# Kernel tuning notes

Hardware: AMD Instinct MI355X
Metric: run time of the kernel (lower is better)

## Reference

```python
import jax, jax.numpy as jnp
import numpy as np


def setup_inputs() -> dict:
    key = jax.random.key(0)
    k1, k2, k3, k4 = jax.random.split(key, 4)
    M, K, N = 16384, 1024, 4096
    # int8-range values stored as int32 (A8W8 path; int32 accumulation is identical)
    x = jax.random.randint(k1, (M, K), -128, 128, dtype=jnp.int32)
    weight = jax.random.randint(k2, (N, K), -128, 128, dtype=jnp.int32)
    scale = jax.random.uniform(k3, (N,), dtype=jnp.float32, minval=0.001, maxval=0.01)
    bias = jax.random.randint(k4, (N,), -64, 64, dtype=jnp.int32)
    return {"x": x, "weight": weight, "scale": scale, "bias": bias}


def reference(x, weight, scale, bias):
    # npu_quant_matmul: int32-accumulated matmul of quantized input with
    # weight^T, int32 bias add, then fused per-out-channel dequant scale.
    acc = jnp.matmul(x, weight.T) + bias[None, :]  # [M, N] int32
    return acc.astype(jnp.float32) * scale[None, :]  # dequantized output
```

## Files before the change

### kernel.cpp

```cpp
#include <hip/hip_runtime.h>

typedef __attribute__((ext_vector_type(4))) int int4v;

#define AS1 __attribute__((address_space(1)))
#define AS3 __attribute__((address_space(3)))

#define BAR()   __builtin_amdgcn_s_barrier()
#define LGKM0() asm volatile("s_waitcnt lgkmcnt(0)" ::: "memory")

#define STG_A(sb, rowbase, k0) \
    __builtin_amdgcn_global_load_lds( \
        (const AS1 void*)(aSrcBase + (size_t)(rowbase) * K + (k0)), \
        (AS3 void*)(ldsDestA + (sb) + (rowbase) * 128), 16, 0, 0)
#define STG_B(sb, rowbase, k0) \
    __builtin_amdgcn_global_load_lds( \
        (const AS1 void*)(bSrcBase + (size_t)(rowbase) * K + (k0)), \
        (AS3 void*)(ldsDestB + (sb) + (rowbase) * 128), 16, 0, 0)

#define LDA(mq, sb) \
    { _Pragma("unroll") for (int m = 0; m < 4; ++m) { \
        const int rb = (sb) + ((aRow0 + ((mq) << 6) + (m << 4)) << 7); \
        a[m][0] = *(const int4v*)(ls + rb + colx0); \
        a[m][1] = *(const int4v*)(ls + rb + colx1); } }

#define LDB(nq, sb) \
    { _Pragma("unroll") for (int n = 0; n < 2; ++n) { \
        const int rb = (sb) + 32768 + ((bRow0 + ((nq) << 5) + (n << 4)) << 7); \
        b[(nq)*2 + n][0] = *(const int4v*)(ls + rb + colx0); \
        b[(nq)*2 + n][1] = *(const int4v*)(ls + rb + colx1); } }

#define MMA(mq, nq) \
    { __builtin_amdgcn_s_setprio(1); \
      _Pragma("unroll") for (int m = 0; m < 4; ++m) \
      _Pragma("unroll") for (int n = 0; n < 2; ++n) { \
        acc[(mq)*4 + m][(nq)*2 + n] = __builtin_amdgcn_mfma_i32_16x16x64_i8( \
            a[m][0], b[(nq)*2 + n][0], acc[(mq)*4 + m][(nq)*2 + n], 0, 0, 0); \
        acc[(mq)*4 + m][(nq)*2 + n] = __builtin_amdgcn_mfma_i32_16x16x64_i8( \
            a[m][1], b[(nq)*2 + n][1], acc[(mq)*4 + m][(nq)*2 + n], 0, 0, 0); } \
      __builtin_amdgcn_s_setprio(0); }

__global__ __launch_bounds__(256) void pack_both_kernel(
    const int* __restrict__ x, const int* __restrict__ w,
    int* __restrict__ x8, int* __restrict__ w8, int n4x, int n4w)
{
    int i = blockIdx.x * blockDim.x + threadIdx.x;
    const int stride = gridDim.x * blockDim.x;
    const int tot = n4x + n4w;
    for (; i < tot; i += stride) {
        const bool isx = i < n4x;
        const int4v v = isx ? ((const int4v*)x)[i] : ((const int4v*)w)[i - n4x];
        const int p = (v.x & 255) | ((v.y & 255) << 8) | ((v.z & 255) << 16) | ((v.w & 255) << 24);
        if (isx) x8[i] = p; else w8[i - n4x] = p;
    }
}

__global__ __launch_bounds__(512, 2) void gemm_i8_256(
    const char* __restrict__ A8, const char* __restrict__ B8,
    const float* __restrict__ scale, const int* __restrict__ bias,
    float* __restrict__ out, int M, int N, int K, int nwg_n)
{
    extern __shared__ __attribute__((aligned(16))) char ls[];

    const int tid  = threadIdx.x;
    const int lane = tid & 63;
    const int wid  = tid >> 6;
    const int wr   = wid >> 2;
    const int wc   = wid & 3;
    const int l15  = lane & 15;
    const int hi16 = lane >> 4;

    int wg = blockIdx.x;
    {
        const int nwg = gridDim.x;
        const int q = nwg >> 3, r = nwg & 7;
        const int x = wg & 7, lq = wg >> 3;
        wg = (x < r ? x * (q + 1) : r * (q + 1) + (x - r) * q) + lq;
    }
    const int m0 = (wg / nwg_n) << 8;
    const int n0 = (wg % nwg_n) << 8;

    const int sw    = (l15 & 7) << 4;
    const int colx0 = ((hi16 << 4)) ^ sw;
    const int colx1 = (64 + (hi16 << 4)) ^ sw;
    const int aRow0 = (wr << 7) + l15;
    const int bRow0 = (wc << 6) + l15;

    const int srow  = tid >> 3;
    const int sslot = tid & 7;
    const int scol  = ((sslot ^ (srow & 7)) << 4);
    const char* aSrcBase = A8 + (size_t)(m0 + srow) * K + scol;
    const char* bSrcBase = B8 + (size_t)(n0 + srow) * K + scol;
    char* ldsDestA = ls + srow * 128 + (sslot << 4);
    char* ldsDestB = ls + 32768 + srow * 128 + (sslot << 4);

    int4v acc[8][4];
#pragma unroll
    for (int i = 0; i < 8; ++i)
#pragma unroll
        for (int j = 0; j < 4; ++j)
            acc[i][j] = (int4v){0, 0, 0, 0};

    int4v a[4][2], b[4][2];

    const int nkt = K >> 7;
    const int nit = nkt >> 1;

    STG_A(0, 0, 0);   STG_A(0, 128, 0);
    STG_A(0, 64, 0);  STG_A(0, 192, 0);
    STG_B(0, 0, 0);   STG_B(0, 64, 0);
    STG_B(0, 128, 0); STG_B(0, 192, 0);
    STG_A(65536, 0, 128); STG_A(65536, 128, 128);
    STG_B(65536, 0, 128); STG_B(65536, 64, 128);
    STG_B(65536, 128, 128); STG_B(65536, 192, 128);
    asm volatile("s_waitcnt vmcnt(6)" ::: "memory");
    BAR();

#pragma unroll 1
    for (int it = 0; it < nit; ++it) {
        const int kO1 = (2 * it + 1) << 7;
        const int tE = 2 * it + 2, tO = 2 * it + 3;
        const int kE = tE << 7, kO = tO << 7;
        const bool ok = tE < nkt;

        LDA(0, 0); LDB(0, 0);
        STG_A(65536, 64, kO1); STG_A(65536, 192, kO1);
        BAR(); LGKM0();
        MMA(0, 0);
        BAR();

        LDB(1, 0);
        if (ok) { STG_A(0, 0, kE); STG_A(0, 128, kE); }
        BAR(); LGKM0();
        MMA(0, 1);
        BAR();

        LDA(1, 0);
        if (ok) { STG_B(0, 0, kE); STG_B(0, 64, kE); }
        BAR(); LGKM0();
        MMA(1, 1);
        BAR();

        if (ok) { STG_B(0, 128, kE); STG_B(0, 192, kE); }
        BAR(); LGKM0();
        MMA(1, 0);
        if (ok) { asm volatile("s_waitcnt vmcnt(6)" ::: "memory"); }
        else    { asm volatile("s_waitcnt vmcnt(0)" ::: "memory"); }
        BAR();

        LDA(0, 65536); LDB(0, 65536);
        if (ok) { STG_A(0, 64, kE); STG_A(0, 192, kE); }
        BAR(); LGKM0();
        MMA(0, 0);
        BAR();

        LDB(1, 65536);
        if (ok) { STG_A(65536, 0, kO); STG_A(65536, 128, kO); }
        BAR(); LGKM0();
        MMA(0, 1);
        BAR();

        LDA(1, 65536);
        if (ok) { STG_B(65536, 0, kO); STG_B(65536, 64, kO); }
        BAR(); LGKM0();
        MMA(1, 1);
        BAR();

        if (ok) { STG_B(65536, 128, kO); STG_B(65536, 192, kO); }
        BAR(); LGKM0();
        MMA(1, 0);
        if (ok) { asm volatile("s_waitcnt vmcnt(6)" ::: "memory"); }
        else    { asm volatile("s_waitcnt vmcnt(0)" ::: "memory"); }
        BAR();
    }

    float scl[4]; int bsv[4];
#pragma unroll
    for (int nj = 0; nj < 4; ++nj) {
        const int col = n0 + (wc << 6) + (nj << 4) + l15;
        scl[nj] = scale[col];
        bsv[nj] = bias[col];
    }
#pragma unroll
    for (int mi = 0; mi < 8; ++mi) {
        const int rowb = m0 + (wr << 7) + (mi << 4) + (hi16 << 2);
#pragma unroll
        for (int nj = 0; nj < 4; ++nj) {
            const int col = n0 + (wc << 6) + (nj << 4) + l15;
            float* o = out + (size_t)rowb * N + col;
#pragma unroll
            for (int r = 0; r < 4; ++r)
                o[(size_t)r * N] = (float)(acc[mi][nj][r] + bsv[nj]) * scl[nj];
        }
    }
}

__global__ __launch_bounds__(256) void naive_kernel(
    const int* __restrict__ x, const int* __restrict__ w,
    const float* __restrict__ scale, const int* __restrict__ bias,
    float* __restrict__ out, int M, int N, int K)
{
    size_t idx = (size_t)blockIdx.x * blockDim.x + threadIdx.x;
    const size_t total = (size_t)M * N;
    const size_t stride = (size_t)gridDim.x * blockDim.x;
    for (; idx < total; idx += stride) {
        const int m = (int)(idx / N), n = (int)(idx % N);
        int acc = 0;
        for (int k = 0; k < K; ++k) acc += x[(size_t)m * K + k] * w[(size_t)n * K + k];
        out[idx] = (float)(acc + bias[n]) * scale[n];
    }
}

extern "C" void kernel_launch(void* const* d_in, const int* in_sizes, int n_in,
                              void* d_out, int out_size, void* d_ws, size_t ws_size,
                              hipStream_t stream)
{
    const int*   x     = (const int*)d_in[0];
    const int*   w     = (const int*)d_in[1];
    const float* scale = (const float*)d_in[2];
    const int*   bias  = (const int*)d_in[3];
    float*       out   = (float*)d_out;

    const int N = in_sizes[2];
    const int K = in_sizes[1] / N;
    const int M = in_sizes[0] / K;

    const size_t needA = (size_t)M * K;
    const size_t needB = (size_t)N * K;

    if (ws_size < needA + needB || (M % 256) || (N % 256) || (K % 256)) {
        naive_kernel<<<8192, 256, 0, stream>>>(x, w, scale, bias, out, M, N, K);
        return;
    }

    char* x8 = (char*)d_ws;
    char* w8 = x8 + needA;

    pack_both_kernel<<<2048, 256, 0, stream>>>(x, w, (int*)x8, (int*)w8,
                                               (int)(needA >> 2), (int)(needB >> 2));

    hipFuncSetAttribute((const void*)gemm_i8_256,
                        hipFuncAttributeMaxDynamicSharedMemorySize, 131072);

    const int nwg_n = N / 256;
    const int nwg = (M / 256) * nwg_n;
    gemm_i8_256<<<nwg, 512, 131072, stream>>>(x8, w8, scale, bias, out, M, N, K, nwg_n);
}
```

Before: 127.9 us.

## Make int8 GEMM persistent with a fixed 256-workgroup grid and chunked tile mapping

Turns the GEMM into a persistent kernel. A grid of at most 256 workgroups loops over the 64x16=1024 output tiles, and each tile restarts its prologue inside the loop. It also replaces the XCD-aware remap with a chunked mapping that gives each of 8 groups a contiguous band of M tiles, aiming for better L2 locality per XCD. Because the grid is 256 workgroups on 256 CUs while 131 KB of LDS allows one resident workgroup per CU, the previous overlap from having many queued workgroups is lost. The tile prologue and epilogue are also no longer overlapped with other work.

```diff
diff --git a/kernel.cpp b/kernel.cpp
--- a/kernel.cpp
+++ b/kernel.cpp
@@ -54,10 +54,11 @@
     }
 }
 
-__global__ __launch_bounds__(512, 2) void gemm_i8_256(
+__global__ __launch_bounds__(512, 2) void gemm_i8_256p(
     const char* __restrict__ A8, const char* __restrict__ B8,
     const float* __restrict__ scale, const int* __restrict__ bias,
-    float* __restrict__ out, int M, int N, int K, int nwg_n)
+    float* __restrict__ out, int M, int N, int K,
+    int mTiles, int nTiles, int chunked)
 {
     extern __shared__ __attribute__((aligned(16))) char ls[];
 
@@ -69,16 +70,6 @@
     const int l15  = lane & 15;
     const int hi16 = lane >> 4;
 
-    int wg = blockIdx.x;
-    {
-        const int nwg = gridDim.x;
-        const int q = nwg >> 3, r = nwg & 7;
-        const int x = wg & 7, lq = wg >> 3;
-        wg = (x < r ? x * (q + 1) : r * (q + 1) + (x - r) * q) + lq;
-    }
-    const int m0 = (wg / nwg_n) << 8;
-    const int n0 = (wg % nwg_n) << 8;
-
     const int sw    = (l15 & 7) << 4;
     const int colx0 = ((hi16 << 4)) ^ sw;
     const int colx1 = (64 + (hi16 << 4)) ^ sw;
@@ -88,108 +79,122 @@
     const int srow  = tid >> 3;
     const int sslot = tid & 7;
     const int scol  = ((sslot ^ (srow & 7)) << 4);
-    const char* aSrcBase = A8 + (size_t)(m0 + srow) * K + scol;
-    const char* bSrcBase = B8 + (size_t)(n0 + srow) * K + scol;
     char* ldsDestA = ls + srow * 128 + (sslot << 4);
     char* ldsDestB = ls + 32768 + srow * 128 + (sslot << 4);
 
-    int4v acc[8][4];
-#pragma unroll
-    for (int i = 0; i < 8; ++i)
-#pragma unroll
-        for (int j = 0; j < 4; ++j)
-            acc[i][j] = (int4v){0, 0, 0, 0};
-
-    int4v a[4][2], b[4][2];
-
     const int nkt = K >> 7;
     const int nit = nkt >> 1;
-
-    STG_A(0, 0, 0);   STG_A(0, 128, 0);
-    STG_A(0, 64, 0);  STG_A(0, 192, 0);
-    STG_B(0, 0, 0);   STG_B(0, 64, 0);
-    STG_B(0, 128, 0); STG_B(0, 192, 0);
-    STG_A(65536, 0, 128); STG_A(65536, 128, 128);
-    STG_B(65536, 0, 128); STG_B(65536, 64, 128);
-    STG_B(65536, 128, 128); STG_B(65536, 192, 128);
-    asm volatile("s_waitcnt vmcnt(6)" ::: "memory");
-    BAR();
+    const int nwg = mTiles * nTiles;
+
+    int4v acc[8][4];
+    int4v a[4][2], b[4][2];
+
+    for (int idx = blockIdx.x; idx < nwg; idx += gridDim.x) {
+        int mt, nt;
+        if (chunked) {
+            const int x = idx & 7, c = idx >> 3;
+            mt = x * (mTiles >> 3) + c / nTiles;
+            nt = c % nTiles;
+        } else {
+            mt = idx / nTiles;
+            nt = idx % nTiles;
+        }
+        const int m0 = mt << 8, n0 = nt << 8;
+        const char* aSrcBase = A8 + (size_t)(m0 + srow) * K + scol;
+        const char* bSrcBase = B8 + (size_t)(n0 + srow) * K + scol;
+
+#pragma unroll
+        for (int i = 0; i < 8; ++i)
+#pragma unroll
+            for (int j = 0; j < 4; ++j)
+                acc[i][j] = (int4v){0, 0, 0, 0};
+
+        STG_A(0, 0, 0);   STG_A(0, 128, 0);
+        STG_A(0, 64, 0);  STG_A(0, 192, 0);
+        STG_B(0, 0, 0);   STG_B(0, 64, 0);
+        STG_B(0, 128, 0); STG_B(0, 192, 0);
+        STG_A(65536, 0, 128); STG_A(65536, 128, 128);
+        STG_B(65536, 0, 128); STG_B(65536, 64, 128);
+        STG_B(65536, 128, 128); STG_B(65536, 192, 128);
+        asm volatile("s_waitcnt vmcnt(6)" ::: "memory");
+        BAR();
 
 #pragma unroll 1
-    for (int it = 0; it < nit; ++it) {
-        const int kO1 = (2 * it + 1) << 7;
-        const int tE = 2 * it + 2, tO = 2 * it + 3;
-        const int kE = tE << 7, kO = tO << 7;
-        const bool ok = tE < nkt;
-
-        LDA(0, 0); LDB(0, 0);
-        STG_A(65536, 64, kO1); STG_A(65536, 192, kO1);
-        BAR(); LGKM0();
-        MMA(0, 0);
-        BAR();
-
-        LDB(1, 0);
-        if (ok) { STG_A(0, 0, kE); STG_A(0, 128, kE); }
-        BAR(); LGKM0();
-        MMA(0, 1);
-        BAR();
-
-        LDA(1, 0);
-        if (ok) { STG_B(0, 0, kE); STG_B(0, 64, kE); }
-        BAR(); LGKM0();
-        MMA(1, 1);
-        BAR();
-
-        if (ok) { STG_B(0, 128, kE); STG_B(0, 192, kE); }
-        BAR(); LGKM0();
-        MMA(1, 0);
-        if (ok) { asm volatile("s_waitcnt vmcnt(6)" ::: "memory"); }
-        else    { asm volatile("s_waitcnt vmcnt(0)" ::: "memory"); }
-        BAR();
-
-        LDA(0, 65536); LDB(0, 65536);
-        if (ok) { STG_A(0, 64, kE); STG_A(0, 192, kE); }
-        BAR(); LGKM0();
-        MMA(0, 0);
-        BAR();
-
-        LDB(1, 65536);
-        if (ok) { STG_A(65536, 0, kO); STG_A(65536, 128, kO); }
-        BAR(); LGKM0();
-        MMA(0, 1);
-        BAR();
-
-        LDA(1, 65536);
-        if (ok) { STG_B(65536, 0, kO); STG_B(65536, 64, kO); }
-        BAR(); LGKM0();
-        MMA(1, 1);
-        BAR();
-
-        if (ok) { STG_B(65536, 128, kO); STG_B(65536, 192, kO); }
-        BAR(); LGKM0();
-        MMA(1, 0);
-        if (ok) { asm volatile("s_waitcnt vmcnt(6)" ::: "memory"); }
-        else    { asm volatile("s_waitcnt vmcnt(0)" ::: "memory"); }
-        BAR();
-    }
-
-    float scl[4]; int bsv[4];
-#pragma unroll
-    for (int nj = 0; nj < 4; ++nj) {
-        const int col = n0 + (wc << 6) + (nj << 4) + l15;
-        scl[nj] = scale[col];
-        bsv[nj] = bias[col];
-    }
-#pragma unroll
-    for (int mi = 0; mi < 8; ++mi) {
-        const int rowb = m0 + (wr << 7) + (mi << 4) + (hi16 << 2);
+        for (int it = 0; it < nit; ++it) {
+            const int kO1 = (2 * it + 1) << 7;
+            const int tE = 2 * it + 2, tO = 2 * it + 3;
+            const int kE = tE << 7, kO = tO << 7;
+            const bool ok = tE < nkt;
+
+            LDA(0, 0); LDB(0, 0);
+            STG_A(65536, 64, kO1); STG_A(65536, 192, kO1);
+            BAR(); LGKM0();
+            MMA(0, 0);
+            BAR();
+
+            LDB(1, 0);
+            if (ok) { STG_A(0, 0, kE); STG_A(0, 128, kE); }
+            BAR(); LGKM0();
+            MMA(0, 1);
+            BAR();
+
+            LDA(1, 0);
+            if (ok) { STG_B(0, 0, kE); STG_B(0, 64, kE); }
+            BAR(); LGKM0();
+            MMA(1, 1);
+            BAR();
+
+            if (ok) { STG_B(0, 128, kE); STG_B(0, 192, kE); }
+            BAR(); LGKM0();
+            MMA(1, 0);
+            if (ok) { asm volatile("s_waitcnt vmcnt(6)" ::: "memory"); }
+            else    { asm volatile("s_waitcnt vmcnt(0)" ::: "memory"); }
+            BAR();
+
+            LDA(0, 65536); LDB(0, 65536);
+            if (ok) { STG_A(0, 64, kE); STG_A(0, 192, kE); }
+            BAR(); LGKM0();
+            MMA(0, 0);
+            BAR();
+
+            LDB(1, 65536);
+            if (ok) { STG_A(65536, 0, kO); STG_A(65536, 128, kO); }
+            BAR(); LGKM0();
+            MMA(0, 1);
+            BAR();
+
+            LDA(1, 65536);
+            if (ok) { STG_B(65536, 0, kO); STG_B(65536, 64, kO); }
+            BAR(); LGKM0();
+            MMA(1, 1);
+            BAR();
+
+            if (ok) { STG_B(65536, 128, kO); STG_B(65536, 192, kO); }
+            BAR(); LGKM0();
+            MMA(1, 0);
+            if (ok) { asm volatile("s_waitcnt vmcnt(6)" ::: "memory"); }
+            else    { asm volatile("s_waitcnt vmcnt(0)" ::: "memory"); }
+            BAR();
+        }
+
+        float scl[4]; int bsv[4];
 #pragma unroll
         for (int nj = 0; nj < 4; ++nj) {
             const int col = n0 + (wc << 6) + (nj << 4) + l15;
-            float* o = out + (size_t)rowb * N + col;
-#pragma unroll
-            for (int r = 0; r < 4; ++r)
-                o[(size_t)r * N] = (float)(acc[mi][nj][r] + bsv[nj]) * scl[nj];
+            scl[nj] = scale[col];
+            bsv[nj] = bias[col];
+        }
+#pragma unroll
+        for (int mi = 0; mi < 8; ++mi) {
+            const int rowb = m0 + (wr << 7) + (mi << 4) + (hi16 << 2);
+#pragma unroll
+            for (int nj = 0; nj < 4; ++nj) {
+                const int col = n0 + (wc << 6) + (nj << 4) + l15;
+                float* o = out + (size_t)rowb * N + col;
+#pragma unroll
+                for (int r = 0; r < 4; ++r)
+                    o[(size_t)r * N] = (float)(acc[mi][nj][r] + bsv[nj]) * scl[nj];
+            }
         }
     }
 }
@@ -238,10 +243,13 @@
     pack_both_kernel<<<2048, 256, 0, stream>>>(x, w, (int*)x8, (int*)w8,
                                                (int)(needA >> 2), (int)(needB >> 2));
 
-    hipFuncSetAttribute((const void*)gemm_i8_256,
+    hipFuncSetAttribute((const void*)gemm_i8_256p,
                         hipFuncAttributeMaxDynamicSharedMemorySize, 131072);
 
-    const int nwg_n = N / 256;
-    const int nwg = (M / 256) * nwg_n;
-    gemm_i8_256<<<nwg, 512, 131072, stream>>>(x8, w8, scale, bias, out, M, N, K, nwg_n);
-}
+    const int mTiles = M / 256, nTiles = N / 256;
+    const int nwg = mTiles * nTiles;
+    const int grid = nwg < 256 ? nwg : 256;
+    const int chunked = (mTiles % 8 == 0) ? 1 : 0;
+    gemm_i8_256p<<<grid, 512, 131072, stream>>>(x8, w8, scale, bias, out,
+                                                M, N, K, mTiles, nTiles, chunked);
+}
```

After: 128.9 us. No clear change (+0.7%).
